# Kernel optimization log

Hardware: AMD Instinct MI355X
Metric: run time of the kernel (lower is better)

The kernel has to match this reference:

```python
import jax, jax.numpy as jnp
import numpy as np

B, CH, H, W = 128, 3, 224, 224
R = 14
S = R * R  # 196 superpixels
DIMS = [11, 96, 192, 384, 768, 768]
BN_EPS = 1e-5


def setup_inputs() -> dict:
    key = jax.random.key(0)
    ks = jax.random.split(key, 64)
    inp = {}
    inp["x"] = jax.random.normal(ks[0], (B, CH, H, W), jnp.float32)
    inp["sliced"] = jax.random.randint(ks[1], (B, H, W), 0, S, jnp.int32)
    ki = 2
    for i in range(5):
        ci, co = DIMS[i], DIMS[i + 1]
        inp[f"w{i}"] = jax.random.normal(ks[ki], (co, ci), jnp.float32) / np.sqrt(ci); ki += 1
        inp[f"b{i}"] = jnp.zeros((co,), jnp.float32)
        inp[f"g{i}"] = jnp.ones((co,), jnp.float32)
        inp[f"be{i}"] = jnp.zeros((co,), jnp.float32)
        inp[f"rm{i}"] = jax.random.normal(ks[ki], (co,), jnp.float32) * 0.1; ki += 1
        inp[f"rv{i}"] = jax.random.uniform(ks[ki], (co,), jnp.float32) + 0.5; ki += 1
    return inp


def _seg_features(x, sliced):
    # x: [B,3,H,W] float, sliced: [B,H,W] int labels in [0,S)
    b, c, h, w = x.shape
    n = h * w
    ids = sliced.reshape(b, n).astype(jnp.int32)
    gid = (jnp.arange(b, dtype=jnp.int32)[:, None] * S + ids).reshape(-1)  # [B*N]

    counts = jax.ops.segment_sum(jnp.ones((b * n,), x.dtype), gid, num_segments=b * S)  # [B*S]
    rows = jnp.repeat(jnp.arange(h, dtype=x.dtype), w)
    cols = jnp.tile(jnp.arange(w, dtype=x.dtype), h)
    coords = jnp.stack([rows, cols], -1)                       # [N,2]
    coords_b = jnp.broadcast_to(coords, (b, n, 2)).reshape(b * n, 2)
    coord_sum = jax.ops.segment_sum(coords_b, gid, num_segments=b * S)  # [B*S,2]

    rgb = x.reshape(b, c, n).transpose(0, 2, 1).reshape(b * n, c)       # [B*N,3]
    rgb_sum = jax.ops.segment_sum(rgb, gid, num_segments=b * S)
    rgb_sq = jax.ops.segment_sum(rgb * rgb, gid, num_segments=b * S)

    cnt = counts[:, None]
    safe = jnp.maximum(cnt, 1.0)
    mean_coord = coord_sum / safe                              # [B*S,2]
    mean_rgb = rgb_sum / safe                                  # [B*S,3]
    # torch .std is unbiased; NaN (count<=1) replaced by 0
    var = (rgb_sq - cnt * mean_rgb * mean_rgb) / jnp.maximum(cnt - 1.0, 1.0)
    std = jnp.where(cnt > 1.0, jnp.sqrt(jnp.maximum(var, 0.0)), 0.0)

    mc = mean_coord.reshape(b, S, 2)
    mr = mean_rgb.reshape(b, S, 3)
    sd = std.reshape(b, S, 3)
    # gather pixel at the (truncated) mean location of each segment
    ri = jnp.clip(mc[..., 0].astype(jnp.int32), 0, h - 1)      # [B,S]
    ci = jnp.clip(mc[..., 1].astype(jnp.int32), 0, w - 1)
    gathered = x[jnp.arange(b)[:, None], :, ri, ci]            # [B,S,3]

    feat = jnp.concatenate([mc, mr, sd, gathered], -1)         # [B,S,11]
    feat = feat * (counts.reshape(b, S, 1) > 0).astype(x.dtype)  # absent segments stay 0
    return feat.transpose(0, 2, 1).reshape(b, 11, R, R)


def _conv_bn(h, w, b, g, be, rm, rv, act):
    # 1x1 conv == channel contraction
    h = jnp.einsum('bchw,oc->bohw', h, w) + b[None, :, None, None]
    scale = g / jnp.sqrt(rv + BN_EPS)
    h = (h - rm[None, :, None, None]) * scale[None, :, None, None] + be[None, :, None, None]
    return jax.nn.relu(h) if act else h


def reference(x, sliced,
              w0, b0, g0, be0, rm0, rv0,
              w1, b1, g1, be1, rm1, rv1,
              w2, b2, g2, be2, rm2, rv2,
              w3, b3, g3, be3, rm3, rv3,
              w4, b4, g4, be4, rm4, rv4):
    params = [(w0, b0, g0, be0, rm0, rv0), (w1, b1, g1, be1, rm1, rv1),
              (w2, b2, g2, be2, rm2, rv2), (w3, b3, g3, be3, rm3, rv3),
              (w4, b4, g4, be4, rm4, rv4)]
    h = _seg_features(x, sliced)                # [B,11,14,14]
    for i, (w, b, g, be, rm, rv) in enumerate(params):
        h = _conv_bn(h, w, b, g, be, rm, rv, act=(i < 4))  # last block: BN only
    return (sliced, h)
```

## Files before the change

### kernel.cpp

```cpp
#include <hip/hip_runtime.h>
#include <hip/hip_bf16.h>

#define HW    50176
#define IMGW  224
#define SEG   196
#define NBATCH 128
#define NCOL  (NBATCH * SEG)
#define PB    14
#define CHUNK (HW / PB)
#define VCHUNK (CHUNK / 4)

typedef __attribute__((ext_vector_type(8))) short bf16x8;
typedef __attribute__((ext_vector_type(4))) float f32x4;
typedef unsigned long long u64;

static __device__ __forceinline__ ushort f2bf(float v) {
    __hip_bfloat16 h = __float2bfloat16(v);
    return *reinterpret_cast<ushort*>(&h);
}

__global__ __launch_bounds__(256) void seg_accum(const float* __restrict__ x,
                                                 const int*   __restrict__ sl,
                                                 float*       __restrict__ stats) {
    __shared__ u64 ls[4][SEG];
    int b    = blockIdx.x / PB;
    int part = blockIdx.x % PB;
    int tid  = threadIdx.x;

    for (int i = tid; i < 4 * SEG; i += 256) (&ls[0][0])[i] = 0ull;
    __syncthreads();

    const float* xb = x + (size_t)b * 3 * HW;
    const int*   sb = sl + (size_t)b * HW;
    int v0 = part * VCHUNK;

    for (int vi = tid; vi < VCHUNK; vi += 256) {
        int vg = v0 + vi;
        int4   id4 = ((const int4*)sb)[vg];
        float4 r4  = ((const float4*)xb)[vg];
        float4 g4  = ((const float4*)(xb + HW))[vg];
        float4 b4  = ((const float4*)(xb + 2 * HW))[vg];
        int p   = vg * 4;
        int row = p / IMGW;
        int col = p - row * IMGW;
        u64 rowbits = ((u64)1 << 48) | ((u64)(unsigned)row << 24);

#pragma unroll
        for (int q = 0; q < 4; ++q) {
            int   id = (q == 0) ? id4.x : (q == 1) ? id4.y : (q == 2) ? id4.z : id4.w;
            float r  = (q == 0) ? r4.x  : (q == 1) ? r4.y  : (q == 2) ? r4.z  : r4.w;
            float g  = (q == 0) ? g4.x  : (q == 1) ? g4.y  : (q == 2) ? g4.z  : g4.w;
            float bl = (q == 0) ? b4.x  : (q == 1) ? b4.y  : (q == 2) ? b4.z  : b4.w;

            unsigned qr  = (unsigned)fmaf(r,  8192.f, 131072.5f);
            unsigned qg  = (unsigned)fmaf(g,  8192.f, 131072.5f);
            unsigned qb  = (unsigned)fmaf(bl, 8192.f, 131072.5f);
            unsigned qr2 = (unsigned)fmaf(r * r,  2048.f, 0.5f);
            unsigned qg2 = (unsigned)fmaf(g * g,  2048.f, 0.5f);
            unsigned qb2 = (unsigned)fmaf(bl * bl, 2048.f, 0.5f);

            atomicAdd(&ls[0][id], rowbits | (unsigned)(col + q));
            atomicAdd(&ls[1][id], ((u64)qg  << 32) | qr);
            atomicAdd(&ls[2][id], ((u64)qr2 << 32) | qb);
            atomicAdd(&ls[3][id], ((u64)qb2 << 32) | qg2);
        }
    }
    __syncthreads();

    const float inv_s = 1.f / 8192.f, inv_q = 1.f / 2048.f;
    for (int i = tid; i < SEG; i += 256) {
        u64 v0p = ls[0][i];
        unsigned cnt = (unsigned)(v0p >> 48);
        if (!cnt) continue;
        float fc   = (float)cnt;
        float rows = (float)((unsigned)(v0p >> 24) & 0xFFFFFFu);
        float cols = (float)((unsigned)v0p & 0xFFFFFFu);
        u64 v1 = ls[1][i], v2 = ls[2][i], v3 = ls[3][i];
        float bias = 16.f * fc;
        float rsum = (float)(unsigned)v1         * inv_s - bias;
        float gsum = (float)(unsigned)(v1 >> 32) * inv_s - bias;
        float bsum = (float)(unsigned)v2         * inv_s - bias;
        float rsq  = (float)(unsigned)(v2 >> 32) * inv_q;
        float gsq  = (float)(unsigned)v3         * inv_q;
        float bsq  = (float)(unsigned)(v3 >> 32) * inv_q;

        size_t base = (size_t)b * SEG + i;
        atomicAdd(&stats[0 * NCOL + base], fc);
        atomicAdd(&stats[1 * NCOL + base], rows);
        atomicAdd(&stats[2 * NCOL + base], cols);
        atomicAdd(&stats[3 * NCOL + base], rsum);
        atomicAdd(&stats[4 * NCOL + base], gsum);
        atomicAdd(&stats[5 * NCOL + base], bsum);
        atomicAdd(&stats[6 * NCOL + base], rsq);
        atomicAdd(&stats[7 * NCOL + base], gsq);
        atomicAdd(&stats[8 * NCOL + base], bsq);
    }
}

__global__ __launch_bounds__(256) void convert_w(const float* __restrict__ src,
                                                 ushort* __restrict__ dst,
                                                 int Cout, int K, int Kpad, int total) {
    int i = blockIdx.x * 256 + threadIdx.x;
    if (i >= total) return;
    int o = i / Kpad, k = i - o * Kpad;
    float v = (o < Cout && k < K) ? src[(size_t)o * K + k] : 0.f;
    dst[i] = f2bf(v);
}

#define SH_W   0
#define SH_F   16384
#define SH_A0  20480
#define SH_A1  28672

__global__ __launch_bounds__(256) void fused_l012(
    const float* __restrict__ x,
    const float* __restrict__ stats,
    const ushort* __restrict__ W0g, const ushort* __restrict__ W1g, const ushort* __restrict__ W2g,
    const float* __restrict__ bias0, const float* __restrict__ gam0, const float* __restrict__ bet0,
    const float* __restrict__ rm0,  const float* __restrict__ rv0,
    const float* __restrict__ bias1, const float* __restrict__ gam1, const float* __restrict__ bet1,
    const float* __restrict__ rm1,  const float* __restrict__ rv1,
    const float* __restrict__ bias2, const float* __restrict__ gam2, const float* __restrict__ bet2,
    const float* __restrict__ rm2,  const float* __restrict__ rv2,
    ushort* __restrict__ outA)
{
    __shared__ ushort sh[45056];
    int tid  = threadIdx.x;
    int lane = tid & 63;
    int wid  = tid >> 6;
    int mrow = lane & 15;
    int quad = lane >> 4;
    int n0   = blockIdx.x * 64;

    if (tid < 64) {
        int r = tid, n = n0 + r;
        float cnt  = stats[n];
        float safe = fmaxf(cnt, 1.f);
        float inv  = 1.f / safe;
        float fmrow = stats[1 * NCOL + n] * inv;
        float fmcol = stats[2 * NCOL + n] * inv;
        float fmr   = stats[3 * NCOL + n] * inv;
        float fmg   = stats[4 * NCOL + n] * inv;
        float fmb   = stats[5 * NCOL + n] * inv;
        float den  = fmaxf(cnt - 1.f, 1.f);
        float vr = (stats[6 * NCOL + n] - cnt * fmr * fmr) / den;
        float vg = (stats[7 * NCOL + n] - cnt * fmg * fmg) / den;
        float vb = (stats[8 * NCOL + n] - cnt * fmb * fmb) / den;
        bool  has2 = cnt > 1.f;
        float sr = has2 ? sqrtf(fmaxf(vr, 0.f)) : 0.f;
        float sg = has2 ? sqrtf(fmaxf(vg, 0.f)) : 0.f;
        float sb = has2 ? sqrtf(fmaxf(vb, 0.f)) : 0.f;
        int b = n / SEG;
        int ri = min(max((int)fmrow, 0), IMGW - 1);
        int ci = min(max((int)fmcol, 0), IMGW - 1);
        const float* xb = x + (size_t)b * 3 * HW;
        int pi = ri * IMGW + ci;
        float gr = xb[pi], gg = xb[HW + pi], gb = xb[2 * HW + pi];
        float mask = cnt > 0.f ? 1.f : 0.f;

        int rx = r & 7;
        bf16x8 v0;
        v0[0] = (short)f2bf(fmrow * mask);
        v0[1] = (short)f2bf(fmcol * mask);
        v0[2] = (short)f2bf(fmr * mask);
        v0[3] = (short)f2bf(fmg * mask);
        v0[4] = (short)f2bf(fmb * mask);
        v0[5] = (short)f2bf(sr * mask);
        v0[6] = (short)f2bf(sg * mask);
        v0[7] = (short)f2bf(sb * mask);
        *(bf16x8*)&sh[SH_F + r * 64 + (0 ^ rx) * 8] = v0;
        bf16x8 v1 = (bf16x8){0,0,0,0,0,0,0,0};
        v1[0] = (short)f2bf(gr * mask);
        v1[1] = (short)f2bf(gg * mask);
        v1[2] = (short)f2bf(gb * mask);
        *(bf16x8*)&sh[SH_F + r * 64 + (1 ^ rx) * 8] = v1;
        bf16x8 z = (bf16x8){0,0,0,0,0,0,0,0};
        for (int g = 2; g < 8; ++g)
            *(bf16x8*)&sh[SH_F + r * 64 + (g ^ rx) * 8] = z;
    }
    __syncthreads();

    auto stageW = [&](int buf, int ot, int kt, const ushort* Wg, int Kl) {
#pragma unroll
        for (int p = 0; p < 4; ++p) {
            int flat = p * 256 + tid;
            int row = flat >> 3, kg = flat & 7;
            int kgs = kg ^ (row & 7);
            const ushort* gp = Wg + (size_t)(ot * 128 + row) * Kl + kt * 64 + kgs * 8;
            __builtin_amdgcn_global_load_lds(
                (const __attribute__((address_space(1))) void*)gp,
                (__attribute__((address_space(3))) void*)&sh[SH_W + buf * 8192 + (p * 256 + wid * 64) * 8],
                16, 0, 0);
        }
    };

    auto run_layer = [&](const ushort* Wg, int KT, int OT, int aOff, int Win,
                         const float* bb, const float* gg_, const float* bbe,
                         const float* rrm, const float* rrv, int CoutL,
                         int outOff, int Wout, int toGlobal, int Kl) {
        stageW(0, 0, 0, Wg, Kl);
        asm volatile("s_waitcnt vmcnt(0)" ::: "memory");
        __builtin_amdgcn_s_barrier();

        int T = OT * KT, cur = 0, ot = 0, kt = 0;
        f32x4 acc[4][2];
        float al[2], bt[2];
        for (int t = 0; t < T; ++t) {
            if (kt == 0) {
#pragma unroll
                for (int j = 0; j < 2; ++j) {
                    acc[0][j] = (f32x4){0.f, 0.f, 0.f, 0.f};
                    acc[1][j] = (f32x4){0.f, 0.f, 0.f, 0.f};
                    acc[2][j] = (f32x4){0.f, 0.f, 0.f, 0.f};
                    acc[3][j] = (f32x4){0.f, 0.f, 0.f, 0.f};
                    int o = ot * 128 + wid * 32 + j * 16 + mrow;
                    float a = 0.f, c = 0.f;
                    if (o < CoutL) {
                        float sc = gg_[o] / sqrtf(rrv[o] + 1e-5f);
                        a = sc;
                        c = (bb[o] - rrm[o]) * sc + bbe[o];
                    }
                    al[j] = a; bt[j] = c;
                }
            }
            if (t + 1 < T) {
                int kt2 = kt + 1, ot2 = ot;
                if (kt2 == KT) { kt2 = 0; ot2 = ot + 1; }
                stageW(cur ^ 1, ot2, kt2, Wg, Kl);
            }
#pragma unroll
            for (int ks = 0; ks < 2; ++ks) {
                bf16x8 af[4], bfr[2];
                int g = kt * 8 + ks * 4 + quad;
#pragma unroll
                for (int i = 0; i < 4; ++i) {
                    int row = i * 16 + mrow;
                    int slot = (g & ~7) | ((g ^ row) & 7);
                    af[i] = *(const bf16x8*)&sh[aOff + row * Win + slot * 8];
                }
#pragma unroll
                for (int j = 0; j < 2; ++j) {
                    int wrow = wid * 32 + j * 16 + mrow;
                    int wslot = (ks * 4 + quad) ^ (wrow & 7);
                    bfr[j] = *(const bf16x8*)&sh[SH_W + cur * 8192 + wrow * 64 + wslot * 8];
                }
#pragma unroll
                for (int i = 0; i < 4; ++i)
#pragma unroll
                    for (int j = 0; j < 2; ++j)
                        acc[i][j] = __builtin_amdgcn_mfma_f32_16x16x32_bf16(af[i], bfr[j], acc[i][j], 0, 0, 0);
            }
            if (t + 1 < T) {
                asm volatile("s_waitcnt vmcnt(0)" ::: "memory");
                __builtin_amdgcn_s_barrier();
            }
            if (kt == KT - 1) {
#pragma unroll
                for (int j = 0; j < 2; ++j) {
                    int o = ot * 128 + wid * 32 + j * 16 + mrow;
#pragma unroll
                    for (int i = 0; i < 4; ++i)
#pragma unroll
                        for (int rr = 0; rr < 4; ++rr) {
                            float v = fmaxf(acc[i][j][rr] * al[j] + bt[j], 0.f);
                            int row = i * 16 + quad * 4 + rr;
                            if (toGlobal) {
                                outA[(size_t)(n0 + row) * 384 + o] = f2bf(v);
                            } else {
                                int cg = o >> 3;
                                int slot = (cg & ~7) | ((cg ^ row) & 7);
                                sh[outOff + row * Wout + slot * 8 + (o & 7)] = f2bf(v);
                            }
                        }
                }
                kt = 0; ++ot;
            } else ++kt;
            cur ^= 1;
        }
        __syncthreads();
    };

    run_layer(W0g, 1, 1, SH_F,  64,  bias0, gam0, bet0, rm0, rv0,  96, SH_A0, 128, 0, 64);
    run_layer(W1g, 2, 2, SH_A0, 128, bias1, gam1, bet1, rm1, rv1, 192, SH_A1, 256, 0, 128);
    run_layer(W2g, 4, 3, SH_A1, 256, bias2, gam2, bet2, rm2, rv2, 384, 0,     384, 1, 256);
}

__global__ __launch_bounds__(256) void gemm_mfma(const ushort* __restrict__ Aact,
                                                 const ushort* __restrict__ Wb,
                                                 void* __restrict__ outp,
                                                 const float* __restrict__ bias,
                                                 const float* __restrict__ gam,
                                                 const float* __restrict__ bet,
                                                 const float* __restrict__ rm,
                                                 const float* __restrict__ rv,
                                                 int Kpad, int Cout, int OutStride,
                                                 int act, int final_out) {
    __shared__ ushort As[2][128 * 64];
    __shared__ ushort Bs[2][128 * 64];

    int tid  = threadIdx.x;
    int lane = tid & 63;
    int wid  = tid >> 6;
    int wm   = wid & 1;
    int wn   = wid >> 1;

    int nbx  = gridDim.x, nby = gridDim.y;
    int nwg  = nbx * nby;
    int orig = blockIdx.y * nbx + blockIdx.x;
    int xcd  = orig & 7;
    int q    = nwg >> 3, r = nwg & 7;
    int wgid = (xcd < r ? xcd * (q + 1) : r * (q + 1) + (xcd - r) * q) + (orig >> 3);
    int bx   = wgid / nby;
    int by   = wgid - bx * nby;
    int n0   = bx * 128;
    int o0   = by * 128;

    int mrow = lane & 15;
    int quad = lane >> 4;
    int swz  = mrow & 7;

    float al4[4], bt4[4];
#pragma unroll
    for (int j = 0; j < 4; ++j) {
        int o = o0 + wn * 64 + j * 16 + mrow;
        float a = 0.f, c = 0.f;
        if (o < Cout) {
            float sc = gam[o] / sqrtf(rv[o] + 1e-5f);
            a = sc;
            c = (bias[o] - rm[o]) * sc + bet[o];
        }
        al4[j] = a; bt4[j] = c;
    }

    f32x4 acc[4][4];
#pragma unroll
    for (int i = 0; i < 4; ++i)
#pragma unroll
        for (int j = 0; j < 4; ++j) acc[i][j] = (f32x4){0.f, 0.f, 0.f, 0.f};

    const ushort* aSrc[4];
    const ushort* bSrc[4];
    int ldsDst[4];
#pragma unroll
    for (int p = 0; p < 4; ++p) {
        int flat = p * 256 + tid;
        int row  = flat >> 3, kg = flat & 7;
        int kgs  = kg ^ (row & 7);
        aSrc[p]  = Aact + (size_t)(n0 + row) * Kpad + kgs * 8;
        bSrc[p]  = Wb   + (size_t)(o0 + row) * Kpad + kgs * 8;
        ldsDst[p] = (p * 256 + wid * 64) * 8;
    }

    auto stage = [&](int buf, int kt) {
        int kb = kt * 64;
#pragma unroll
        for (int p = 0; p < 4; ++p)
            __builtin_amdgcn_global_load_lds(
                (const __attribute__((address_space(1))) void*)(aSrc[p] + kb),
                (__attribute__((address_space(3))) void*)(&As[buf][ldsDst[p]]),
                16, 0, 0);
#pragma unroll
        for (int p = 0; p < 4; ++p)
            __builtin_amdgcn_global_load_lds(
                (const __attribute__((address_space(1))) void*)(bSrc[p] + kb),
                (__attribute__((address_space(3))) void*)(&Bs[buf][ldsDst[p]]),
                16, 0, 0);
    };

    auto compute = [&](int buf) {
#pragma unroll
        for (int ks = 0; ks < 2; ++ks) {
            bf16x8 af[4], bfr[4];
            int gbase = ks * 4 + quad;
            int slot  = (gbase ^ swz) * 8;
#pragma unroll
            for (int i = 0; i < 4; ++i)
                af[i] = *(const bf16x8*)&As[buf][(size_t)(wm * 64 + i * 16 + mrow) * 64 + slot];
#pragma unroll
            for (int j = 0; j < 4; ++j)
                bfr[j] = *(const bf16x8*)&Bs[buf][(size_t)(wn * 64 + j * 16 + mrow) * 64 + slot];
#pragma unroll
            for (int i = 0; i < 4; ++i)
#pragma unroll
                for (int j = 0; j < 4; ++j)
                    acc[i][j] = __builtin_amdgcn_mfma_f32_16x16x32_bf16(af[i], bfr[j], acc[i][j], 0, 0, 0);
        }
    };

    int ktiles = Kpad >> 6;

    stage(0, 0);
    asm volatile("s_waitcnt vmcnt(0)" ::: "memory");
    __builtin_amdgcn_s_barrier();

    int cur = 0;
    for (int t = 0; t < ktiles - 1; ++t) {
        stage(cur ^ 1, t + 1);
        compute(cur);
        asm volatile("s_waitcnt vmcnt(0)" ::: "memory");
        __builtin_amdgcn_s_barrier();
        cur ^= 1;
    }
    compute(cur);

#pragma unroll
    for (int j = 0; j < 4; ++j) {
        int o = o0 + wn * 64 + j * 16 + mrow;
#pragma unroll
        for (int i = 0; i < 4; ++i) {
            int nbase = n0 + wm * 64 + i * 16 + quad * 4;
#pragma unroll
            for (int rr = 0; rr < 4; ++rr) {
                float v = acc[i][j][rr] * al4[j] + bt4[j];
                if (act) v = fmaxf(v, 0.f);
                int n = nbase + rr;
                if (final_out) {
                    int b = n / SEG, s = n - b * SEG;
                    ((float*)outp)[(size_t)b * 768 * SEG + (size_t)o * SEG + s] = v;
                } else {
                    ((ushort*)outp)[(size_t)n * OutStride + o] = f2bf(v);
                }
            }
        }
    }
}

__global__ __launch_bounds__(256) void copy_sliced(const int4* __restrict__ sl,
                                                   float4* __restrict__ out) {
    int i = blockIdx.x * 256 + threadIdx.x;
    int4 v = sl[i];
    out[i] = make_float4((float)v.x, (float)v.y, (float)v.z, (float)v.w);
}

extern "C" void kernel_launch(void* const* d_in, const int* in_sizes, int n_in,
                              void* d_out, int out_size, void* d_ws, size_t ws_size,
                              hipStream_t stream) {
    const float* x  = (const float*)d_in[0];
    const int*   sl = (const int*)d_in[1];
    const float* Wp[5], *Bp[5], *Gp[5], *BEp[5], *RMp[5], *RVp[5];
    for (int i = 0; i < 5; ++i) {
        Wp[i]  = (const float*)d_in[2 + 6 * i + 0];
        Bp[i]  = (const float*)d_in[2 + 6 * i + 1];
        Gp[i]  = (const float*)d_in[2 + 6 * i + 2];
        BEp[i] = (const float*)d_in[2 + 6 * i + 3];
        RMp[i] = (const float*)d_in[2 + 6 * i + 4];
        RVp[i] = (const float*)d_in[2 + 6 * i + 5];
    }
    float* out = (float*)d_out;

    const int Kpad[5]  = {64, 128, 256, 384, 768};
    const int Kreal[5] = {11, 96, 192, 384, 768};
    const int Cout[5]  = {96, 192, 384, 768, 768};
    const int Opad[5]  = {128, 256, 384, 768, 768};

    char* wsb = (char*)d_ws;
    float*  stats = (float*)wsb;
    wsb += (size_t)9 * NCOL * sizeof(float);
    ushort* F = (ushort*)wsb;
    wsb += (size_t)NCOL * 64 * sizeof(ushort);
    ushort* Wpad[5];
    for (int i = 0; i < 5; ++i) {
        Wpad[i] = (ushort*)wsb;
        wsb += (size_t)Opad[i] * Kpad[i] * sizeof(ushort);
    }
    ushort* bufA = (ushort*)wsb;
    wsb += (size_t)NCOL * 384 * sizeof(ushort);
    ushort* bufB = (ushort*)wsb;
    (void)F;

    hipMemsetAsync(stats, 0, (size_t)9 * NCOL * sizeof(float), stream);

    for (int i = 0; i < 5; ++i) {
        int total = Opad[i] * Kpad[i];
        convert_w<<<(total + 255) / 256, 256, 0, stream>>>(
            Wp[i], Wpad[i], Cout[i], Kreal[i], Kpad[i], total);
    }

    seg_accum<<<NBATCH * PB, 256, 0, stream>>>(x, sl, stats);

    fused_l012<<<NCOL / 64, 256, 0, stream>>>(
        x, stats, Wpad[0], Wpad[1], Wpad[2],
        Bp[0], Gp[0], BEp[0], RMp[0], RVp[0],
        Bp[1], Gp[1], BEp[1], RMp[1], RVp[1],
        Bp[2], Gp[2], BEp[2], RMp[2], RVp[2],
        bufA);

    const int NT = NCOL / 128;
    gemm_mfma<<<dim3(NT, Opad[3] / 128), 256, 0, stream>>>(
        bufA, Wpad[3], bufB, Bp[3], Gp[3], BEp[3], RMp[3], RVp[3],
        Kpad[3], Cout[3], Opad[3], 1, 0);
    gemm_mfma<<<dim3(NT, Opad[4] / 128), 256, 0, stream>>>(
        bufB, Wpad[4], out + (size_t)NBATCH * HW, Bp[4], Gp[4], BEp[4], RMp[4], RVp[4],
        Kpad[4], Cout[4], 0, 0, 1);

    copy_sliced<<<(NBATCH * HW / 4) / 256, 256, 0, stream>>>((const int4*)sl,
                                                             (float4*)out);
}
```

Before: 411.0 us.

## Fuse sliced copy into seg_accum, batch weight conversion, simplify GEMM to single buffer

Measured after the change: 401.3 us. -2.4%, faster.

```diff
diff --git a/kernel.cpp b/kernel.cpp
--- a/kernel.cpp
+++ b/kernel.cpp
@@ -21,7 +21,8 @@
 
 __global__ __launch_bounds__(256) void seg_accum(const float* __restrict__ x,
                                                  const int*   __restrict__ sl,
-                                                 float*       __restrict__ stats) {
+                                                 float*       __restrict__ stats,
+                                                 float*       __restrict__ outf) {
     __shared__ u64 ls[4][SEG];
     int b    = blockIdx.x / PB;
     int part = blockIdx.x % PB;
@@ -32,6 +33,7 @@
 
     const float* xb = x + (size_t)b * 3 * HW;
     const int*   sb = sl + (size_t)b * HW;
+    float4*      ob = (float4*)(outf + (size_t)b * HW);
     int v0 = part * VCHUNK;
 
     for (int vi = tid; vi < VCHUNK; vi += 256) {
@@ -40,6 +42,9 @@
         float4 r4  = ((const float4*)xb)[vg];
         float4 g4  = ((const float4*)(xb + HW))[vg];
         float4 b4  = ((const float4*)(xb + 2 * HW))[vg];
+
+        ob[vg] = make_float4((float)id4.x, (float)id4.y, (float)id4.z, (float)id4.w);
+
         int p   = vg * 4;
         int row = p / IMGW;
         int col = p - row * IMGW;
@@ -97,11 +102,20 @@
     }
 }
 
-__global__ __launch_bounds__(256) void convert_w(const float* __restrict__ src,
-                                                 ushort* __restrict__ dst,
-                                                 int Cout, int K, int Kpad, int total) {
-    int i = blockIdx.x * 256 + threadIdx.x;
-    if (i >= total) return;
+__global__ __launch_bounds__(256) void convert_all(
+    const float* __restrict__ s0, const float* __restrict__ s1,
+    const float* __restrict__ s2, const float* __restrict__ s3,
+    const float* __restrict__ s4,
+    ushort* __restrict__ d0, ushort* __restrict__ d1, ushort* __restrict__ d2,
+    ushort* __restrict__ d3, ushort* __restrict__ d4) {
+    int blk = blockIdx.x;
+    const float* src; ushort* dst; int Cout, K, Kpad, base;
+    if (blk < 32)        { src = s0; dst = d0; Cout = 96;  K = 11;  Kpad = 64;  base = 0;    }
+    else if (blk < 160)  { src = s1; dst = d1; Cout = 192; K = 96;  Kpad = 128; base = 32;   }
+    else if (blk < 544)  { src = s2; dst = d2; Cout = 384; K = 192; Kpad = 256; base = 160;  }
+    else if (blk < 1696) { src = s3; dst = d3; Cout = 768; K = 384; Kpad = 384; base = 544;  }
+    else                 { src = s4; dst = d4; Cout = 768; K = 768; Kpad = 768; base = 1696; }
+    int i = (blk - base) * 256 + threadIdx.x;
     int o = i / Kpad, k = i - o * Kpad;
     float v = (o < Cout && k < K) ? src[(size_t)o * K + k] : 0.f;
     dst[i] = f2bf(v);
@@ -295,79 +309,53 @@
                                                  const float* __restrict__ rv,
                                                  int Kpad, int Cout, int OutStride,
                                                  int act, int final_out) {
-    __shared__ ushort As[2][128 * 64];
-    __shared__ ushort Bs[2][128 * 64];
+    __shared__ ushort As[128 * 64];
+    __shared__ ushort Bs[128 * 64];
 
     int tid  = threadIdx.x;
     int lane = tid & 63;
     int wid  = tid >> 6;
     int wm   = wid & 1;
     int wn   = wid >> 1;
-
-    int nbx  = gridDim.x, nby = gridDim.y;
-    int nwg  = nbx * nby;
-    int orig = blockIdx.y * nbx + blockIdx.x;
-    int xcd  = orig & 7;
-    int q    = nwg >> 3, r = nwg & 7;
-    int wgid = (xcd < r ? xcd * (q + 1) : r * (q + 1) + (xcd - r) * q) + (orig >> 3);
-    int bx   = wgid / nby;
-    int by   = wgid - bx * nby;
-    int n0   = bx * 128;
-    int o0   = by * 128;
-
+    int n0   = blockIdx.x * 128;
+    int o0   = blockIdx.y * 128;
     int mrow = lane & 15;
     int quad = lane >> 4;
     int swz  = mrow & 7;
 
-    float al4[4], bt4[4];
-#pragma unroll
-    for (int j = 0; j < 4; ++j) {
-        int o = o0 + wn * 64 + j * 16 + mrow;
-        float a = 0.f, c = 0.f;
-        if (o < Cout) {
-            float sc = gam[o] / sqrtf(rv[o] + 1e-5f);
-            a = sc;
-            c = (bias[o] - rm[o]) * sc + bet[o];
-        }
-        al4[j] = a; bt4[j] = c;
-    }
-
     f32x4 acc[4][4];
 #pragma unroll
     for (int i = 0; i < 4; ++i)
 #pragma unroll
         for (int j = 0; j < 4; ++j) acc[i][j] = (f32x4){0.f, 0.f, 0.f, 0.f};
 
-    const ushort* aSrc[4];
-    const ushort* bSrc[4];
-    int ldsDst[4];
-#pragma unroll
-    for (int p = 0; p < 4; ++p) {
-        int flat = p * 256 + tid;
-        int row  = flat >> 3, kg = flat & 7;
-        int kgs  = kg ^ (row & 7);
-        aSrc[p]  = Aact + (size_t)(n0 + row) * Kpad + kgs * 8;
-        bSrc[p]  = Wb   + (size_t)(o0 + row) * Kpad + kgs * 8;
-        ldsDst[p] = (p * 256 + wid * 64) * 8;
-    }
-
-    auto stage = [&](int buf, int kt) {
+    int ktiles = Kpad >> 6;
+    for (int kt = 0; kt < ktiles; ++kt) {
         int kb = kt * 64;
 #pragma unroll
-        for (int p = 0; p < 4; ++p)
+        for (int p = 0; p < 4; ++p) {
+            int flat = p * 256 + tid;
+            int row = flat >> 3, kg = flat & 7;
+            int kgs = kg ^ (row & 7);
+            const ushort* gp = Aact + (size_t)(n0 + row) * Kpad + kb + kgs * 8;
             __builtin_amdgcn_global_load_lds(
-                (const __attribute__((address_space(1))) void*)(aSrc[p] + kb),
-                (__attribute__((address_space(3))) void*)(&As[buf][ldsDst[p]]),
+                (const __attribute__((address_space(1))) void*)gp,
+                (__attribute__((address_space(3))) void*)(As + (size_t)(p * 256 + wid * 64) * 8),
                 16, 0, 0);
-#pragma unroll
-        for (int p = 0; p < 4; ++p)
+        }
+#pragma unroll
+        for (int p = 0; p < 4; ++p) {
+            int flat = p * 256 + tid;
+            int row = flat >> 3, kg = flat & 7;
+            int kgs = kg ^ (row & 7);
+            const ushort* gp = Wb + (size_t)(o0 + row) * Kpad + kb + kgs * 8;
             __builtin_amdgcn_global_load_lds(
-                (const __attribute__((address_space(1))) void*)(bSrc[p] + kb),
-                (__attribute__((address_space(3))) void*)(&Bs[buf][ldsDst[p]]),
+                (const __attribute__((address_space(1))) void*)gp,
+                (__attribute__((address_space(3))) void*)(Bs + (size_t)(p * 256 + wid * 64) * 8),
                 16, 0, 0);
-    };
-
-    auto compute = [&](int buf) {
+        }
+        __syncthreads();
+
 #pragma unroll
         for (int ks = 0; ks < 2; ++ks) {
             bf16x8 af[4], bfr[4];
@@ -375,45 +363,36 @@
             int slot  = (gbase ^ swz) * 8;
 #pragma unroll
             for (int i = 0; i < 4; ++i)
-                af[i] = *(const bf16x8*)&As[buf][(size_t)(wm * 64 + i * 16 + mrow) * 64 + slot];
+                af[i] = *(const bf16x8*)&As[(size_t)(wm * 64 + i * 16 + mrow) * 64 + slot];
 #pragma unroll
             for (int j = 0; j < 4; ++j)
-                bfr[j] = *(const bf16x8*)&Bs[buf][(size_t)(wn * 64 + j * 16 + mrow) * 64 + slot];
+                bfr[j] = *(const bf16x8*)&Bs[(size_t)(wn * 64 + j * 16 + mrow) * 64 + slot];
 #pragma unroll
             for (int i = 0; i < 4; ++i)
 #pragma unroll
                 for (int j = 0; j < 4; ++j)
                     acc[i][j] = __builtin_amdgcn_mfma_f32_16x16x32_bf16(af[i], bfr[j], acc[i][j], 0, 0, 0);
         }
-    };
-
-    int ktiles = Kpad >> 6;
-
-    stage(0, 0);
-    asm volatile("s_waitcnt vmcnt(0)" ::: "memory");
-    __builtin_amdgcn_s_barrier();
-
-    int cur = 0;
-    for (int t = 0; t < ktiles - 1; ++t) {
-        stage(cur ^ 1, t + 1);
-        compute(cur);
-        asm volatile("s_waitcnt vmcnt(0)" ::: "memory");
-        __builtin_amdgcn_s_barrier();
-        cur ^= 1;
-    }
-    compute(cur);
+        __syncthreads();
+    }
 
 #pragma unroll
     for (int j = 0; j < 4; ++j) {
         int o = o0 + wn * 64 + j * 16 + mrow;
+        float al = 0.f, bt = 0.f;
+        if (o < Cout) {
+            float sc = gam[o] / sqrtf(rv[o] + 1e-5f);
+            al = sc;
+            bt = (bias[o] - rm[o]) * sc + bet[o];
+        }
 #pragma unroll
         for (int i = 0; i < 4; ++i) {
             int nbase = n0 + wm * 64 + i * 16 + quad * 4;
 #pragma unroll
-            for (int rr = 0; rr < 4; ++rr) {
-                float v = acc[i][j][rr] * al4[j] + bt4[j];
+            for (int r = 0; r < 4; ++r) {
+                float v = acc[i][j][r] * al + bt;
                 if (act) v = fmaxf(v, 0.f);
-                int n = nbase + rr;
+                int n = nbase + r;
                 if (final_out) {
                     int b = n / SEG, s = n - b * SEG;
                     ((float*)outp)[(size_t)b * 768 * SEG + (size_t)o * SEG + s] = v;
@@ -423,13 +402,6 @@
             }
         }
     }
-}
-
-__global__ __launch_bounds__(256) void copy_sliced(const int4* __restrict__ sl,
-                                                   float4* __restrict__ out) {
-    int i = blockIdx.x * 256 + threadIdx.x;
-    int4 v = sl[i];
-    out[i] = make_float4((float)v.x, (float)v.y, (float)v.z, (float)v.w);
 }
 
 extern "C" void kernel_launch(void* const* d_in, const int* in_sizes, int n_in,
@@ -449,7 +421,6 @@
     float* out = (float*)d_out;
 
     const int Kpad[5]  = {64, 128, 256, 384, 768};
-    const int Kreal[5] = {11, 96, 192, 384, 768};
     const int Cout[5]  = {96, 192, 384, 768, 768};
     const int Opad[5]  = {128, 256, 384, 768, 768};
 
@@ -470,13 +441,11 @@
 
     hipMemsetAsync(stats, 0, (size_t)9 * NCOL * sizeof(float), stream);
 
-    for (int i = 0; i < 5; ++i) {
-        int total = Opad[i] * Kpad[i];
-        convert_w<<<(total + 255) / 256, 256, 0, stream>>>(
-            Wp[i], Wpad[i], Cout[i], Kreal[i], Kpad[i], total);
-    }
-
-    seg_accum<<<NBATCH * PB, 256, 0, stream>>>(x, sl, stats);
+    convert_all<<<4000, 256, 0, stream>>>(
+        Wp[0], Wp[1], Wp[2], Wp[3], Wp[4],
+        Wpad[0], Wpad[1], Wpad[2], Wpad[3], Wpad[4]);
+
+    seg_accum<<<NBATCH * PB, 256, 0, stream>>>(x, sl, stats, out);
 
     fused_l012<<<NCOL / 64, 256, 0, stream>>>(
         x, stats, Wpad[0], Wpad[1], Wpad[2],
@@ -492,7 +461,4 @@
     gemm_mfma<<<dim3(NT, Opad[4] / 128), 256, 0, stream>>>(
         bufB, Wpad[4], out + (size_t)NBATCH * HW, Bp[4], Gp[4], BEp[4], RMp[4], RVp[4],
         Kpad[4], Cout[4], 0, 0, 1);
-
-    copy_sliced<<<(NBATCH * HW / 4) / 256, 256, 0, stream>>>((const int4*)sl,
-                                                             (float4*)out);
-}
+}
```
